# Performance work log

Measured on AMD Instinct MI355X. Metric: run time of the kernel, lower is better.

Reference implementation:

```python
import jax, jax.numpy as jnp
import numpy as np

B, N, L, D, H = 32, 512, 1024, 512, 8
C = D // H  # 64 channels per head
SCALE = C ** -0.5


def setup_inputs() -> dict:
    key = jax.random.key(0)
    ks = jax.random.split(key, 10)
    inp = {
        "x_q": jax.random.normal(ks[0], (B, N, D), dtype=jnp.float32),
        "x_kv": jax.random.normal(ks[1], (B, L, D), dtype=jnp.float32),
        "pad_mask": jax.random.randint(ks[2], (B, L), 0, 2).astype(bool),
        # projection weights stored (in, out); no bias except o_proj
        "Wq": jax.random.normal(ks[3], (D, D), dtype=jnp.float32) * (D ** -0.5),
        "Wk": jax.random.normal(ks[4], (D, D), dtype=jnp.float32) * (D ** -0.5),
        "Wv": jax.random.normal(ks[5], (D, D), dtype=jnp.float32) * (D ** -0.5),
        "Wo": jax.random.normal(ks[6], (D, D), dtype=jnp.float32) * (D ** -0.5),
        "bo": jnp.zeros((D,), dtype=jnp.float32),
        # relative position bias, shape (1, feat_w*feat_h, num_qk_channels)
        "rpb": jax.random.normal(ks[7], (1, L, D), dtype=jnp.float32) * 0.02,
    }
    return inp


def reference(x_q, x_kv, pad_mask, Wq, Wk, Wv, Wo, bo, rpb):
    # linear projections
    q = jnp.einsum("bnd,de->bne", x_q, Wq)
    k = jnp.einsum("bld,de->ble", x_kv, Wk) + rpb  # rel-pos bias added to K
    v = jnp.einsum("bld,de->ble", x_kv, Wv)
    # split heads: (B, S, H*C) -> (B, H, S, C)
    split = lambda t: t.reshape(t.shape[0], t.shape[1], H, C).transpose(0, 2, 1, 3)
    q, k, v = split(q), split(k), split(v)
    attn = jnp.einsum("bhic,bhjc->bhij", q, k) * SCALE  # (B,H,N,L)
    neg = -jnp.finfo(attn.dtype).max
    attn = jnp.where(pad_mask[:, None, None, :], neg, attn)
    attn = jax.nn.softmax(attn, axis=-1)
    o = jnp.einsum("bhij,bhjc->bhic", attn, v)
    o = o.transpose(0, 2, 1, 3).reshape(B, N, H * C)  # merge heads
    return jnp.einsum("bnd,de->bne", o, Wo) + bo
```

## Files before the change

### kernel.cpp

```cpp
#include <hip/hip_runtime.h>
#include <hip/hip_bf16.h>

typedef __hip_bfloat16 bf16;
typedef __attribute__((ext_vector_type(8))) short short8;
typedef __attribute__((ext_vector_type(4))) float f32x4;
typedef __attribute__((ext_vector_type(16))) float f32x16;

#define B_SZ 32
#define N_SZ 512
#define L_SZ 1024
#define D_SZ 512
#define H_SZ 8

__device__ __forceinline__ void gload16(void* lds, const void* g) {
    typedef const __attribute__((address_space(1))) unsigned int* gp_t;
    typedef __attribute__((address_space(3))) unsigned int* lp_t;
    __builtin_amdgcn_global_load_lds((gp_t)g, (lp_t)lds, 16, 0, 0);
}

__device__ __forceinline__ unsigned int cvtpk(float lo, float hi) {
    unsigned int r;
    asm("v_cvt_pk_bf16_f32 %0, %1, %2" : "=v"(r) : "v"(lo), "v"(hi));
    return r;
}

__device__ __forceinline__ float fexp2(float x) {
    float r;
    asm("v_exp_f32 %0, %1" : "=v"(r) : "v"(x));
    return r;
}

struct alignas(8) B4 { bf16 a, b, c, d; };

__global__ void cvt4(const float* __restrict__ s, bf16* __restrict__ d, int n4) {
    int i = blockIdx.x * 256 + threadIdx.x;
    if (i < n4) {
        float4 v = ((const float4*)s)[i];
        B4 o;
        o.a = __float2bfloat16(v.x);
        o.b = __float2bfloat16(v.y);
        o.c = __float2bfloat16(v.z);
        o.d = __float2bfloat16(v.w);
        *(B4*)(d + (size_t)i * 4) = o;
    }
}

__global__ void tpose4(const float* __restrict__ s0, const float* __restrict__ s1,
                       const float* __restrict__ s2, const float* __restrict__ s3,
                       bf16* __restrict__ d0, bf16* __restrict__ d1,
                       bf16* __restrict__ d2, bf16* __restrict__ d3) {
    __shared__ float t[32][33];
    const float* s = blockIdx.z == 0 ? s0 : blockIdx.z == 1 ? s1 : blockIdx.z == 2 ? s2 : s3;
    bf16* d = blockIdx.z == 0 ? d0 : blockIdx.z == 1 ? d1 : blockIdx.z == 2 ? d2 : d3;
    int tx = threadIdx.x, ty = threadIdx.y;
    int r0 = blockIdx.y * 32, c0 = blockIdx.x * 32;
#pragma unroll
    for (int i = 0; i < 32; i += 8)
        t[ty + i][tx] = s[(size_t)(r0 + ty + i) * 512 + c0 + tx];
    __syncthreads();
#pragma unroll
    for (int i = 0; i < 32; i += 8)
        d[(size_t)(c0 + ty + i) * 512 + r0 + tx] = __float2bfloat16(t[tx][ty + i]);
}

template <int MODE>
__global__ __launch_bounds__(256) void gemm512(const bf16* __restrict__ A,
                                               const bf16* __restrict__ Bt,
                                               void* __restrict__ outp,
                                               const float* __restrict__ bias, int logS) {
    __shared__ bf16 lA[128 * 64];
    __shared__ bf16 lB[128 * 64];
    const int tid = threadIdx.x;
    const int wave = tid >> 6, lane = tid & 63;
    const int wr = wave >> 1, wc = wave & 1;
    const int g16 = lane >> 4, r16 = lane & 15;
    const long rowBase = (long)blockIdx.x * 128;
    const int colBase = blockIdx.y * 128;

    f32x4 acc[4][4];
#pragma unroll
    for (int m = 0; m < 4; ++m)
#pragma unroll
        for (int n = 0; n < 4; ++n) acc[m][n] = {0.f, 0.f, 0.f, 0.f};

    for (int k0 = 0; k0 < 512; k0 += 64) {
        __syncthreads();
#pragma unroll
        for (int rnd = 0; rnd < 4; ++rnd) {
            int chunk = rnd * 256 + tid;
            int row = chunk >> 3, j = chunk & 7, gj = j ^ (row & 7);
            gload16((char*)lA + chunk * 16, A + (rowBase + row) * 512 + k0 + gj * 8);
            gload16((char*)lB + chunk * 16, Bt + (long)(colBase + row) * 512 + k0 + gj * 8);
        }
        __syncthreads();
#pragma unroll
        for (int kk = 0; kk < 2; ++kk) {
            short8 a[4], b[4];
#pragma unroll
            for (int m = 0; m < 4; ++m) {
                int row = wr * 64 + m * 16 + r16;
                a[m] = *(const short8*)((const char*)lA + row * 128 +
                                        (((kk * 4 + g16) ^ (row & 7)) * 16));
            }
#pragma unroll
            for (int n = 0; n < 4; ++n) {
                int row = wc * 64 + n * 16 + r16;
                b[n] = *(const short8*)((const char*)lB + row * 128 +
                                        (((kk * 4 + g16) ^ (row & 7)) * 16));
            }
#pragma unroll
            for (int m = 0; m < 4; ++m)
#pragma unroll
                for (int n = 0; n < 4; ++n)
                    acc[m][n] =
                        __builtin_amdgcn_mfma_f32_16x16x32_bf16(a[m], b[n], acc[m][n], 0, 0, 0);
        }
    }

    const int S = 1 << logS;
#pragma unroll
    for (int m = 0; m < 4; ++m) {
#pragma unroll
        for (int r = 0; r < 4; ++r) {
            long gm = rowBase + wr * 64 + m * 16 + g16 * 4 + r;
            if (MODE == 2) {
                int e = (int)gm;
                int h = e >> 6, c = e & 63;
#pragma unroll
                for (int n = 0; n < 4; ++n) {
                    int gl = colBase + wc * 64 + n * 16 + r16;
                    int bb = gl >> 10, s = gl & 1023;
                    long idx = (((long)bb * H_SZ + h) * 64 + c) * (long)L_SZ + s;
                    ((bf16*)outp)[idx] = __float2bfloat16(acc[m][n][r]);
                }
            } else {
                int bb = (int)(gm >> logS);
                int s = (int)gm & (S - 1);
#pragma unroll
                for (int n = 0; n < 4; ++n) {
                    int e = colBase + wc * 64 + n * 16 + r16;
                    float v = acc[m][n][r];
                    if (MODE == 1) v += bias[(long)s * 512 + e];
                    if (MODE == 3) {
                        ((float*)outp)[gm * 512 + e] = v + bias[e];
                    } else {
                        int h = e >> 6, c = e & 63;
                        long idx = (((long)bb * H_SZ + h) * (long)S + s) * 64 + c;
                        ((bf16*)outp)[idx] = __float2bfloat16(v);
                    }
                }
            }
        }
    }
}

__global__ __launch_bounds__(512, 4) void attn256(const bf16* __restrict__ q,
                                                  const bf16* __restrict__ k,
                                                  const bf16* __restrict__ vT,
                                                  const int* __restrict__ mask,
                                                  bf16* __restrict__ o) {
    __shared__ bf16 lK[2][32 * 64];
    __shared__ bf16 lV[2][64 * 32];
    __shared__ float lMf[1024];

    const int tid = threadIdx.x;
    const int wv = tid >> 6, lane = tid & 63;
    const int q32 = lane & 31, hi = lane >> 5;

    const int wg = blockIdx.x;
    const int xcd = wg & 7, slot = wg >> 3;
    const int bh = xcd * 32 + (slot >> 1), qc = slot & 1;
    const int b = bh >> 3, h = bh & 7;

    const bf16* kbase = k + (long)bh * L_SZ * 64;
    const bf16* vbase = vT + (long)bh * 64 * L_SZ;

    const int* mrow = mask + b * L_SZ;
    lMf[tid] = mrow[tid] ? -1e38f : 0.f;
    lMf[tid + 512] = mrow[tid + 512] ? -1e38f : 0.f;

    const bf16* gsrc;
    int gstep;
    char *dst0, *dst1;
    {
        int sc = (wv & 3) * 64 + lane;
        if (wv < 4) {
            int r = sc >> 3, j = sc & 7, gj = j ^ (r & 7);
            gsrc = kbase + r * 64 + gj * 8;
            gstep = 32 * 64;
            dst0 = (char*)(&lK[0][0]) + wv * 1024;
            dst1 = (char*)(&lK[1][0]) + wv * 1024;
        } else {
            int c = sc >> 2, j = sc & 3, gj = j ^ (c & 3);
            gsrc = vbase + (long)c * L_SZ + gj * 8;
            gstep = 32;
            dst0 = (char*)(&lV[0][0]) + (wv - 4) * 1024;
            dst1 = (char*)(&lV[1][0]) + (wv - 4) * 1024;
        }
    }
    gload16(dst0, gsrc);

    const bf16* qp = q + ((long)bh * N_SZ + qc * 256 + wv * 32 + q32) * 64 + hi * 8;
    short8 qf[4];
#pragma unroll
    for (int t = 0; t < 4; ++t) qf[t] = *(const short8*)(qp + t * 16);

    float mrun = 0.f, lrun = 0.f;
    f32x16 oa0, oa1;
#pragma unroll
    for (int i = 0; i < 16; ++i) { oa0[i] = 0.f; oa1[i] = 0.f; }

    __syncthreads();

    const float CL = 0.18033688011112042f;

    for (int kb = 0; kb < 32; ++kb) {
        const char* curK = (const char*)(&lK[kb & 1][0]);
        const char* curV = (const char*)(&lV[kb & 1][0]);
        if (kb < 31) gload16((kb & 1) ? dst0 : dst1, gsrc + (long)(kb + 1) * gstep);

        f32x16 s;
#pragma unroll
        for (int i = 0; i < 16; ++i) s[i] = 0.f;
#pragma unroll
        for (int t = 0; t < 4; ++t) {
            short8 kf = *(const short8*)(curK + q32 * 128 + (((t * 2 + hi) ^ (q32 & 7)) * 16));
            s = __builtin_amdgcn_mfma_f32_32x32x16_bf16(kf, qf[t], s, 0, 0, 0);
        }

        const float* mf = lMf + kb * 32 + hi * 4;
        float4 mq0 = *(const float4*)(mf);
        float4 mq1 = *(const float4*)(mf + 8);
        float4 mq2 = *(const float4*)(mf + 16);
        float4 mq3 = *(const float4*)(mf + 24);
        float mb[16] = {mq0.x, mq0.y, mq0.z, mq0.w, mq1.x, mq1.y, mq1.z, mq1.w,
                        mq2.x, mq2.y, mq2.z, mq2.w, mq3.x, mq3.y, mq3.z, mq3.w};

        float t16[16];
#pragma unroll
        for (int i = 0; i < 16; ++i) t16[i] = fmaf(s[i], CL, mb[i]);

        float m8[8];
#pragma unroll
        for (int i = 0; i < 8; ++i) m8[i] = fmaxf(t16[i], t16[i + 8]);
        float tm = fmaxf(fmaxf(fmaxf(m8[0], m8[4]), fmaxf(m8[1], m8[5])),
                         fmaxf(fmaxf(m8[2], m8[6]), fmaxf(m8[3], m8[7])));
        tm = fmaxf(tm, __shfl_xor(tm, 32));

        if (__any(tm > mrun + 8.f)) {
            float mnew = fmaxf(mrun, tm);
            float al = fexp2(mrun - mnew);
            mrun = mnew;
            lrun *= al;
#pragma unroll
            for (int i = 0; i < 16; ++i) { oa0[i] *= al; oa1[i] *= al; }
        }

#pragma unroll
        for (int i = 0; i < 16; ++i) t16[i] = fexp2(t16[i] - mrun);
        float s8[8];
#pragma unroll
        for (int i = 0; i < 8; ++i) s8[i] = t16[i] + t16[i + 8];
        float ps = ((s8[0] + s8[4]) + (s8[1] + s8[5])) + ((s8[2] + s8[6]) + (s8[3] + s8[7]));
        ps += __shfl_xor(ps, 32);
        lrun += ps;

        unsigned int x0 = cvtpk(t16[0], t16[1]), x1 = cvtpk(t16[2], t16[3]),
                     x2 = cvtpk(t16[4], t16[5]), x3 = cvtpk(t16[6], t16[7]),
                     x4 = cvtpk(t16[8], t16[9]), x5 = cvtpk(t16[10], t16[11]),
                     x6 = cvtpk(t16[12], t16[13]), x7 = cvtpk(t16[14], t16[15]);
        asm("v_permlane32_swap_b32 %0, %1" : "+v"(x0), "+v"(x2));
        asm("v_permlane32_swap_b32 %0, %1" : "+v"(x1), "+v"(x3));
        asm("v_permlane32_swap_b32 %0, %1" : "+v"(x4), "+v"(x6));
        asm("v_permlane32_swap_b32 %0, %1" : "+v"(x5), "+v"(x7));
        union U { unsigned int u[4]; short8 s8v; };
        U f1, f2;
        f1.u[0] = x0; f1.u[1] = x1; f1.u[2] = x2; f1.u[3] = x3;
        f2.u[0] = x4; f2.u[1] = x5; f2.u[2] = x6; f2.u[3] = x7;

#pragma unroll
        for (int kt = 0; kt < 2; ++kt) {
            short8 pf = kt ? f2.s8v : f1.s8v;
            int sw = ((kt * 2 + hi) ^ (q32 & 3)) * 16;
            short8 v0 = *(const short8*)(curV + (q32)*64 + sw);
            short8 v1 = *(const short8*)(curV + (32 + q32) * 64 + sw);
            oa0 = __builtin_amdgcn_mfma_f32_32x32x16_bf16(v0, pf, oa0, 0, 0, 0);
            oa1 = __builtin_amdgcn_mfma_f32_32x32x16_bf16(v1, pf, oa1, 0, 0, 0);
        }

        __syncthreads();
    }

    float inv = 1.f / lrun;
    bf16* op = o + ((long)b * N_SZ + qc * 256 + wv * 32 + q32) * 512 + h * 64;
#pragma unroll
    for (int ct = 0; ct < 2; ++ct) {
#pragma unroll
        for (int rq = 0; rq < 4; ++rq) {
            int c0 = ct * 32 + rq * 8 + hi * 4;
            float v0 = (ct ? oa1[rq * 4 + 0] : oa0[rq * 4 + 0]) * inv;
            float v1 = (ct ? oa1[rq * 4 + 1] : oa0[rq * 4 + 1]) * inv;
            float v2 = (ct ? oa1[rq * 4 + 2] : oa0[rq * 4 + 2]) * inv;
            float v3 = (ct ? oa1[rq * 4 + 3] : oa0[rq * 4 + 3]) * inv;
            uint2 st;
            st.x = cvtpk(v0, v1);
            st.y = cvtpk(v2, v3);
            *(uint2*)(op + c0) = st;
        }
    }
}

extern "C" void kernel_launch(void* const* d_in, const int* in_sizes, int n_in,
                              void* d_out, int out_size, void* d_ws, size_t ws_size,
                              hipStream_t stream) {
    const float* x_q  = (const float*)d_in[0];
    const float* x_kv = (const float*)d_in[1];
    const int*   mask = (const int*)d_in[2];
    const float* Wq   = (const float*)d_in[3];
    const float* Wk   = (const float*)d_in[4];
    const float* Wv   = (const float*)d_in[5];
    const float* Wo   = (const float*)d_in[6];
    const float* bo   = (const float*)d_in[7];
    const float* rpb  = (const float*)d_in[8];
    float* out = (float*)d_out;

    char* w = (char*)d_ws;
    bf16* xq_bf  = (bf16*)(w + 0);
    bf16* xkv_bf = (bf16*)(w + 16777216);
    bf16* WqT    = (bf16*)(w + 50331648);
    bf16* WkT    = WqT + 262144;
    bf16* WvT    = WkT + 262144;
    bf16* WoT    = WvT + 262144;
    bf16* qh     = (bf16*)(w + 52428800);
    bf16* kh     = (bf16*)(w + 69206016);
    bf16* vTh    = (bf16*)(w + 102760448);
    bf16* o_bf   = xq_bf;

    cvt4<<<8192, 256, 0, stream>>>(x_q, xq_bf, 2097152);
    cvt4<<<16384, 256, 0, stream>>>(x_kv, xkv_bf, 4194304);
    tpose4<<<dim3(16, 16, 4), dim3(32, 8), 0, stream>>>(Wq, Wk, Wv, Wo, WqT, WkT, WvT, WoT);

    gemm512<0><<<dim3(128, 4), 256, 0, stream>>>(xq_bf, WqT, qh, nullptr, 9);
    gemm512<1><<<dim3(256, 4), 256, 0, stream>>>(xkv_bf, WkT, kh, rpb, 10);
    gemm512<2><<<dim3(4, 256), 256, 0, stream>>>(WvT, xkv_bf, vTh, nullptr, 10);

    attn256<<<512, 512, 0, stream>>>(qh, kh, vTh, mask, o_bf);

    gemm512<3><<<dim3(128, 4), 256, 0, stream>>>(o_bf, WoT, out, bo, 9);
}
```

Before: 187.7 us.

## Merge launches and widen attention key tile to 64 per iteration

Merges the two fp32-to-bf16 conversion kernels into one launch and the three Q/K/V projection GEMMs into a single grid that selects its mode by block index, cutting launch count and tail gaps. The attention kernel now processes 64 keys per iteration instead of 32, with every thread loading both K and V tiles. This halves the loop trips and barriers and gives more MFMA work between syncs. In exchange it doubles LDS per block and raises register pressure, which may lower occupancy under launch_bounds(512,4).

```diff
diff --git a/kernel.cpp b/kernel.cpp
--- a/kernel.cpp
+++ b/kernel.cpp
@@ -32,17 +32,23 @@
 
 struct alignas(8) B4 { bf16 a, b, c, d; };
 
-__global__ void cvt4(const float* __restrict__ s, bf16* __restrict__ d, int n4) {
+__global__ void cvt_all(const float* __restrict__ xq, const float* __restrict__ xkv,
+                        bf16* __restrict__ dq, bf16* __restrict__ dkv) {
     int i = blockIdx.x * 256 + threadIdx.x;
-    if (i < n4) {
-        float4 v = ((const float4*)s)[i];
-        B4 o;
-        o.a = __float2bfloat16(v.x);
-        o.b = __float2bfloat16(v.y);
-        o.c = __float2bfloat16(v.z);
-        o.d = __float2bfloat16(v.w);
-        *(B4*)(d + (size_t)i * 4) = o;
-    }
+    const float* s;
+    bf16* d;
+    if (i < 2097152) {
+        s = xq; d = dq;
+    } else {
+        i -= 2097152; s = xkv; d = dkv;
+    }
+    float4 v = ((const float4*)s)[i];
+    B4 o;
+    o.a = __float2bfloat16(v.x);
+    o.b = __float2bfloat16(v.y);
+    o.c = __float2bfloat16(v.z);
+    o.d = __float2bfloat16(v.w);
+    *(B4*)(d + (size_t)i * 4) = o;
 }
 
 __global__ void tpose4(const float* __restrict__ s0, const float* __restrict__ s1,
@@ -63,11 +69,116 @@
         d[(size_t)(c0 + ty + i) * 512 + r0 + tx] = __float2bfloat16(t[tx][ty + i]);
 }
 
-template <int MODE>
-__global__ __launch_bounds__(256) void gemm512(const bf16* __restrict__ A,
-                                               const bf16* __restrict__ Bt,
-                                               void* __restrict__ outp,
-                                               const float* __restrict__ bias, int logS) {
+__global__ __launch_bounds__(256) void gemm_qkv(
+    const bf16* __restrict__ xq, const bf16* __restrict__ xkv,
+    const bf16* __restrict__ WqT, const bf16* __restrict__ WkT,
+    const bf16* __restrict__ WvT, const float* __restrict__ rpb,
+    bf16* __restrict__ qh, bf16* __restrict__ kh, bf16* __restrict__ vTh) {
+    __shared__ bf16 lA[128 * 64];
+    __shared__ bf16 lB[128 * 64];
+    const int tid = threadIdx.x;
+    const int wave = tid >> 6, lane = tid & 63;
+    const int wr = wave >> 1, wc = wave & 1;
+    const int g16 = lane >> 4, r16 = lane & 15;
+
+    int bid = blockIdx.x;
+    int mode;
+    long rowBase;
+    int colBase;
+    const bf16 *A, *Bt;
+    if (bid < 512) {
+        mode = 0; A = xq; Bt = WqT;
+        rowBase = (long)(bid >> 2) * 128; colBase = (bid & 3) * 128;
+    } else if (bid < 1536) {
+        mode = 1; int t = bid - 512; A = xkv; Bt = WkT;
+        rowBase = (long)(t >> 2) * 128; colBase = (t & 3) * 128;
+    } else {
+        mode = 2; int t = bid - 1536; A = WvT; Bt = xkv;
+        rowBase = (long)(t & 3) * 128; colBase = (t >> 2) * 128;
+    }
+
+    f32x4 acc[4][4];
+#pragma unroll
+    for (int m = 0; m < 4; ++m)
+#pragma unroll
+        for (int n = 0; n < 4; ++n) acc[m][n] = {0.f, 0.f, 0.f, 0.f};
+
+    for (int k0 = 0; k0 < 512; k0 += 64) {
+        __syncthreads();
+#pragma unroll
+        for (int rnd = 0; rnd < 4; ++rnd) {
+            int chunk = rnd * 256 + tid;
+            int row = chunk >> 3, j = chunk & 7, gj = j ^ (row & 7);
+            gload16((char*)lA + chunk * 16, A + (rowBase + row) * 512 + k0 + gj * 8);
+            gload16((char*)lB + chunk * 16, Bt + (long)(colBase + row) * 512 + k0 + gj * 8);
+        }
+        __syncthreads();
+#pragma unroll
+        for (int kk = 0; kk < 2; ++kk) {
+            short8 a[4], b[4];
+#pragma unroll
+            for (int m = 0; m < 4; ++m) {
+                int row = wr * 64 + m * 16 + r16;
+                a[m] = *(const short8*)((const char*)lA + row * 128 +
+                                        (((kk * 4 + g16) ^ (row & 7)) * 16));
+            }
+#pragma unroll
+            for (int n = 0; n < 4; ++n) {
+                int row = wc * 64 + n * 16 + r16;
+                b[n] = *(const short8*)((const char*)lB + row * 128 +
+                                        (((kk * 4 + g16) ^ (row & 7)) * 16));
+            }
+#pragma unroll
+            for (int m = 0; m < 4; ++m)
+#pragma unroll
+                for (int n = 0; n < 4; ++n)
+                    acc[m][n] =
+                        __builtin_amdgcn_mfma_f32_16x16x32_bf16(a[m], b[n], acc[m][n], 0, 0, 0);
+        }
+    }
+
+#pragma unroll
+    for (int m = 0; m < 4; ++m) {
+#pragma unroll
+        for (int r = 0; r < 4; ++r) {
+            long gm = rowBase + wr * 64 + m * 16 + g16 * 4 + r;
+            if (mode == 2) {
+                int e = (int)gm;
+                int hh = e >> 6, c = e & 63;
+#pragma unroll
+                for (int n = 0; n < 4; ++n) {
+                    int gl = colBase + wc * 64 + n * 16 + r16;
+                    int bb = gl >> 10, s = gl & 1023;
+                    vTh[(((long)bb * H_SZ + hh) * 64 + c) * (long)L_SZ + s] =
+                        __float2bfloat16(acc[m][n][r]);
+                }
+            } else if (mode == 1) {
+                int bb = (int)(gm >> 10), s = (int)gm & 1023;
+#pragma unroll
+                for (int n = 0; n < 4; ++n) {
+                    int e = colBase + wc * 64 + n * 16 + r16;
+                    float v = acc[m][n][r] + rpb[(long)s * 512 + e];
+                    int hh = e >> 6, c = e & 63;
+                    kh[(((long)bb * H_SZ + hh) * (long)L_SZ + s) * 64 + c] = __float2bfloat16(v);
+                }
+            } else {
+                int bb = (int)(gm >> 9), s = (int)gm & 511;
+#pragma unroll
+                for (int n = 0; n < 4; ++n) {
+                    int e = colBase + wc * 64 + n * 16 + r16;
+                    int hh = e >> 6, c = e & 63;
+                    qh[(((long)bb * H_SZ + hh) * (long)N_SZ + s) * 64 + c] =
+                        __float2bfloat16(acc[m][n][r]);
+                }
+            }
+        }
+    }
+}
+
+__global__ __launch_bounds__(256) void gemm_o(const bf16* __restrict__ A,
+                                              const bf16* __restrict__ Bt,
+                                              float* __restrict__ outp,
+                                              const float* __restrict__ bias) {
     __shared__ bf16 lA[128 * 64];
     __shared__ bf16 lB[128 * 64];
     const int tid = threadIdx.x;
@@ -117,38 +228,15 @@
         }
     }
 
-    const int S = 1 << logS;
 #pragma unroll
     for (int m = 0; m < 4; ++m) {
 #pragma unroll
         for (int r = 0; r < 4; ++r) {
             long gm = rowBase + wr * 64 + m * 16 + g16 * 4 + r;
-            if (MODE == 2) {
-                int e = (int)gm;
-                int h = e >> 6, c = e & 63;
-#pragma unroll
-                for (int n = 0; n < 4; ++n) {
-                    int gl = colBase + wc * 64 + n * 16 + r16;
-                    int bb = gl >> 10, s = gl & 1023;
-                    long idx = (((long)bb * H_SZ + h) * 64 + c) * (long)L_SZ + s;
-                    ((bf16*)outp)[idx] = __float2bfloat16(acc[m][n][r]);
-                }
-            } else {
-                int bb = (int)(gm >> logS);
-                int s = (int)gm & (S - 1);
-#pragma unroll
-                for (int n = 0; n < 4; ++n) {
-                    int e = colBase + wc * 64 + n * 16 + r16;
-                    float v = acc[m][n][r];
-                    if (MODE == 1) v += bias[(long)s * 512 + e];
-                    if (MODE == 3) {
-                        ((float*)outp)[gm * 512 + e] = v + bias[e];
-                    } else {
-                        int h = e >> 6, c = e & 63;
-                        long idx = (((long)bb * H_SZ + h) * (long)S + s) * 64 + c;
-                        ((bf16*)outp)[idx] = __float2bfloat16(v);
-                    }
-                }
+#pragma unroll
+            for (int n = 0; n < 4; ++n) {
+                int e = colBase + wc * 64 + n * 16 + r16;
+                outp[gm * 512 + e] = acc[m][n][r] + bias[e];
             }
         }
     }
@@ -159,8 +247,8 @@
                                                   const bf16* __restrict__ vT,
                                                   const int* __restrict__ mask,
                                                   bf16* __restrict__ o) {
-    __shared__ bf16 lK[2][32 * 64];
-    __shared__ bf16 lV[2][64 * 32];
+    __shared__ bf16 lK[2][64 * 64];
+    __shared__ bf16 lV[2][64 * 64];
     __shared__ float lMf[1024];
 
     const int tid = threadIdx.x;
@@ -179,26 +267,16 @@
     lMf[tid] = mrow[tid] ? -1e38f : 0.f;
     lMf[tid + 512] = mrow[tid + 512] ? -1e38f : 0.f;
 
-    const bf16* gsrc;
-    int gstep;
-    char *dst0, *dst1;
-    {
-        int sc = (wv & 3) * 64 + lane;
-        if (wv < 4) {
-            int r = sc >> 3, j = sc & 7, gj = j ^ (r & 7);
-            gsrc = kbase + r * 64 + gj * 8;
-            gstep = 32 * 64;
-            dst0 = (char*)(&lK[0][0]) + wv * 1024;
-            dst1 = (char*)(&lK[1][0]) + wv * 1024;
-        } else {
-            int c = sc >> 2, j = sc & 3, gj = j ^ (c & 3);
-            gsrc = vbase + (long)c * L_SZ + gj * 8;
-            gstep = 32;
-            dst0 = (char*)(&lV[0][0]) + (wv - 4) * 1024;
-            dst1 = (char*)(&lV[1][0]) + (wv - 4) * 1024;
-        }
-    }
-    gload16(dst0, gsrc);
+    const int r_ = tid >> 3, j_ = tid & 7;
+    const int gj_ = (j_ ^ (r_ & 7)) * 8;
+    const bf16* gK = kbase + r_ * 64 + gj_;
+    const bf16* gV = vbase + (long)r_ * L_SZ + gj_;
+    char* dK0 = (char*)(&lK[0][0]) + tid * 16;
+    char* dK1 = (char*)(&lK[1][0]) + tid * 16;
+    char* dV0 = (char*)(&lV[0][0]) + tid * 16;
+    char* dV1 = (char*)(&lV[1][0]) + tid * 16;
+    gload16(dK0, gK);
+    gload16(dV0, gV);
 
     const bf16* qp = q + ((long)bh * N_SZ + qc * 256 + wv * 32 + q32) * 64 + hi * 8;
     short8 qf[4];
@@ -214,35 +292,53 @@
 
     const float CL = 0.18033688011112042f;
 
-    for (int kb = 0; kb < 32; ++kb) {
+    for (int kb = 0; kb < 16; ++kb) {
         const char* curK = (const char*)(&lK[kb & 1][0]);
         const char* curV = (const char*)(&lV[kb & 1][0]);
-        if (kb < 31) gload16((kb & 1) ? dst0 : dst1, gsrc + (long)(kb + 1) * gstep);
-
-        f32x16 s;
-#pragma unroll
-        for (int i = 0; i < 16; ++i) s[i] = 0.f;
+        if (kb < 15) {
+            gload16((kb & 1) ? dK0 : dK1, gK + (kb + 1) * 4096);
+            gload16((kb & 1) ? dV0 : dV1, gV + (kb + 1) * 64);
+        }
+
+        f32x16 sA, sB;
+#pragma unroll
+        for (int i = 0; i < 16; ++i) { sA[i] = 0.f; sB[i] = 0.f; }
 #pragma unroll
         for (int t = 0; t < 4; ++t) {
-            short8 kf = *(const short8*)(curK + q32 * 128 + (((t * 2 + hi) ^ (q32 & 7)) * 16));
-            s = __builtin_amdgcn_mfma_f32_32x32x16_bf16(kf, qf[t], s, 0, 0, 0);
-        }
-
-        const float* mf = lMf + kb * 32 + hi * 4;
-        float4 mq0 = *(const float4*)(mf);
-        float4 mq1 = *(const float4*)(mf + 8);
-        float4 mq2 = *(const float4*)(mf + 16);
-        float4 mq3 = *(const float4*)(mf + 24);
-        float mb[16] = {mq0.x, mq0.y, mq0.z, mq0.w, mq1.x, mq1.y, mq1.z, mq1.w,
-                        mq2.x, mq2.y, mq2.z, mq2.w, mq3.x, mq3.y, mq3.z, mq3.w};
-
-        float t16[16];
-#pragma unroll
-        for (int i = 0; i < 16; ++i) t16[i] = fmaf(s[i], CL, mb[i]);
-
+            int sl = ((t * 2 + hi) ^ (q32 & 7)) * 16;
+            short8 kfA = *(const short8*)(curK + q32 * 128 + sl);
+            short8 kfB = *(const short8*)(curK + (32 + q32) * 128 + sl);
+            sA = __builtin_amdgcn_mfma_f32_32x32x16_bf16(kfA, qf[t], sA, 0, 0, 0);
+            sB = __builtin_amdgcn_mfma_f32_32x32x16_bf16(kfB, qf[t], sB, 0, 0, 0);
+        }
+
+        const float* mf = lMf + kb * 64 + hi * 4;
+        float4 ma0 = *(const float4*)(mf);
+        float4 ma1 = *(const float4*)(mf + 8);
+        float4 ma2 = *(const float4*)(mf + 16);
+        float4 ma3 = *(const float4*)(mf + 24);
+        float4 mb0 = *(const float4*)(mf + 32);
+        float4 mb1 = *(const float4*)(mf + 40);
+        float4 mb2 = *(const float4*)(mf + 48);
+        float4 mb3 = *(const float4*)(mf + 56);
+        float mba[16] = {ma0.x, ma0.y, ma0.z, ma0.w, ma1.x, ma1.y, ma1.z, ma1.w,
+                         ma2.x, ma2.y, ma2.z, ma2.w, ma3.x, ma3.y, ma3.z, ma3.w};
+        float mbb[16] = {mb0.x, mb0.y, mb0.z, mb0.w, mb1.x, mb1.y, mb1.z, mb1.w,
+                         mb2.x, mb2.y, mb2.z, mb2.w, mb3.x, mb3.y, mb3.z, mb3.w};
+
+        float t32[32];
+#pragma unroll
+        for (int i = 0; i < 16; ++i) {
+            t32[i] = fmaf(sA[i], CL, mba[i]);
+            t32[16 + i] = fmaf(sB[i], CL, mbb[i]);
+        }
+
+        float m16[16];
+#pragma unroll
+        for (int i = 0; i < 16; ++i) m16[i] = fmaxf(t32[i], t32[16 + i]);
         float m8[8];
 #pragma unroll
-        for (int i = 0; i < 8; ++i) m8[i] = fmaxf(t16[i], t16[i + 8]);
+        for (int i = 0; i < 8; ++i) m8[i] = fmaxf(m16[i], m16[i + 8]);
         float tm = fmaxf(fmaxf(fmaxf(m8[0], m8[4]), fmaxf(m8[1], m8[5])),
                          fmaxf(fmaxf(m8[2], m8[6]), fmaxf(m8[3], m8[7])));
         tm = fmaxf(tm, __shfl_xor(tm, 32));
@@ -257,35 +353,38 @@
         }
 
 #pragma unroll
-        for (int i = 0; i < 16; ++i) t16[i] = fexp2(t16[i] - mrun);
+        for (int i = 0; i < 32; ++i) t32[i] = fexp2(t32[i] - mrun);
+        float s16[16];
+#pragma unroll
+        for (int i = 0; i < 16; ++i) s16[i] = t32[i] + t32[16 + i];
         float s8[8];
 #pragma unroll
-        for (int i = 0; i < 8; ++i) s8[i] = t16[i] + t16[i + 8];
+        for (int i = 0; i < 8; ++i) s8[i] = s16[i] + s16[i + 8];
         float ps = ((s8[0] + s8[4]) + (s8[1] + s8[5])) + ((s8[2] + s8[6]) + (s8[3] + s8[7]));
         ps += __shfl_xor(ps, 32);
         lrun += ps;
 
-        unsigned int x0 = cvtpk(t16[0], t16[1]), x1 = cvtpk(t16[2], t16[3]),
-                     x2 = cvtpk(t16[4], t16[5]), x3 = cvtpk(t16[6], t16[7]),
-                     x4 = cvtpk(t16[8], t16[9]), x5 = cvtpk(t16[10], t16[11]),
-                     x6 = cvtpk(t16[12], t16[13]), x7 = cvtpk(t16[14], t16[15]);
-        asm("v_permlane32_swap_b32 %0, %1" : "+v"(x0), "+v"(x2));
-        asm("v_permlane32_swap_b32 %0, %1" : "+v"(x1), "+v"(x3));
-        asm("v_permlane32_swap_b32 %0, %1" : "+v"(x4), "+v"(x6));
-        asm("v_permlane32_swap_b32 %0, %1" : "+v"(x5), "+v"(x7));
         union U { unsigned int u[4]; short8 s8v; };
-        U f1, f2;
-        f1.u[0] = x0; f1.u[1] = x1; f1.u[2] = x2; f1.u[3] = x3;
-        f2.u[0] = x4; f2.u[1] = x5; f2.u[2] = x6; f2.u[3] = x7;
-
-#pragma unroll
-        for (int kt = 0; kt < 2; ++kt) {
-            short8 pf = kt ? f2.s8v : f1.s8v;
-            int sw = ((kt * 2 + hi) ^ (q32 & 3)) * 16;
-            short8 v0 = *(const short8*)(curV + (q32)*64 + sw);
-            short8 v1 = *(const short8*)(curV + (32 + q32) * 64 + sw);
-            oa0 = __builtin_amdgcn_mfma_f32_32x32x16_bf16(v0, pf, oa0, 0, 0, 0);
-            oa1 = __builtin_amdgcn_mfma_f32_32x32x16_bf16(v1, pf, oa1, 0, 0, 0);
+        U fr[4];
+#pragma unroll
+        for (int fkt = 0; fkt < 4; ++fkt) {
+            const float* tp = t32 + fkt * 8;
+            unsigned int y0 = cvtpk(tp[0], tp[1]);
+            unsigned int y1 = cvtpk(tp[2], tp[3]);
+            unsigned int y2 = cvtpk(tp[4], tp[5]);
+            unsigned int y3 = cvtpk(tp[6], tp[7]);
+            asm("v_permlane32_swap_b32 %0, %1" : "+v"(y0), "+v"(y2));
+            asm("v_permlane32_swap_b32 %0, %1" : "+v"(y1), "+v"(y3));
+            fr[fkt].u[0] = y0; fr[fkt].u[1] = y1; fr[fkt].u[2] = y2; fr[fkt].u[3] = y3;
+        }
+
+#pragma unroll
+        for (int kt = 0; kt < 4; ++kt) {
+            int sw = ((kt * 2 + hi) ^ (q32 & 7)) * 16;
+            short8 v0 = *(const short8*)(curV + q32 * 128 + sw);
+            short8 v1 = *(const short8*)(curV + (32 + q32) * 128 + sw);
+            oa0 = __builtin_amdgcn_mfma_f32_32x32x16_bf16(v0, fr[kt].s8v, oa0, 0, 0, 0);
+            oa1 = __builtin_amdgcn_mfma_f32_32x32x16_bf16(v1, fr[kt].s8v, oa1, 0, 0, 0);
         }
 
         __syncthreads();
@@ -336,15 +435,12 @@
     bf16* vTh    = (bf16*)(w + 102760448);
     bf16* o_bf   = xq_bf;
 
-    cvt4<<<8192, 256, 0, stream>>>(x_q, xq_bf, 2097152);
-    cvt4<<<16384, 256, 0, stream>>>(x_kv, xkv_bf, 4194304);
+    cvt_all<<<24576, 256, 0, stream>>>(x_q, x_kv, xq_bf, xkv_bf);
     tpose4<<<dim3(16, 16, 4), dim3(32, 8), 0, stream>>>(Wq, Wk, Wv, Wo, WqT, WkT, WvT, WoT);
 
-    gemm512<0><<<dim3(128, 4), 256, 0, stream>>>(xq_bf, WqT, qh, nullptr, 9);
-    gemm512<1><<<dim3(256, 4), 256, 0, stream>>>(xkv_bf, WkT, kh, rpb, 10);
-    gemm512<2><<<dim3(4, 256), 256, 0, stream>>>(WvT, xkv_bf, vTh, nullptr, 10);
+    gemm_qkv<<<2560, 256, 0, stream>>>(xq_bf, xkv_bf, WqT, WkT, WvT, rpb, qh, kh, vTh);
 
     attn256<<<512, 512, 0, stream>>>(qh, kh, vTh, mask, o_bf);
 
-    gemm512<3><<<dim3(128, 4), 256, 0, stream>>>(o_bf, WoT, out, bo, 9);
-}
+    gemm_o<<<dim3(128, 4), 256, 0, stream>>>(o_bf, WoT, out, bo);
+}
```

After: 184.7 us. About the same (-1.6%).
